# Performance work log

Hardware: AMD Instinct MI355X
Metric: run time of the kernel (lower is better)

The kernel has to match this reference:

```python
import jax, jax.numpy as jnp
import numpy as np

D_MODEL = 1024
N_HEADS = 16
D_HEAD = 64
NEG = -1000000000.0


def setup_inputs() -> dict:
    key = jax.random.key(0)
    k1, k2, k3 = jax.random.split(key, 3)
    B, T = 2, 2048
    x = jax.random.normal(k1, (B, T, D_MODEL), dtype=jnp.float32)
    # qkv_proj: Linear(d_model, 3*H*D, bias=False) -> weight (3*H*D, d_model)
    w_qkv = jax.random.normal(k2, (3 * N_HEADS * D_HEAD, D_MODEL), dtype=jnp.float32) * (D_MODEL ** -0.5)
    # o_proj: Linear(H*D, d_model, bias=False) -> weight (d_model, H*D)
    w_o = jax.random.normal(k3, (D_MODEL, N_HEADS * D_HEAD), dtype=jnp.float32) * ((N_HEADS * D_HEAD) ** -0.5)
    return {"x": x, "w_qkv": w_qkv, "w_o": w_o}


def reference(x, w_qkv, w_o):
    B, T, _ = x.shape
    H, D = N_HEADS, D_HEAD
    scale = D ** -0.5
    qkv = jnp.einsum('btm,nm->btn', x, w_qkv).reshape(B, T, 3, H, D)
    q, k, v = qkv[:, :, 0], qkv[:, :, 1], qkv[:, :, 2]  # (B,T,H,D)
    # scores: (B,H,T,T)
    attn = jnp.einsum('bqhd,bkhd->bhqk', q, k) * scale
    causal = jnp.tril(jnp.ones((T, T), dtype=x.dtype))
    attn = attn + (1.0 - causal) * NEG
    attn = jax.nn.softmax(attn, axis=-1)
    out = jnp.einsum('bhqk,bkhd->bqhd', attn, v).reshape(B, T, H * D)
    out = jnp.einsum('btn,mn->btm', out, w_o)
    return (out, k, v)
```

## Files before the change

### kernel.cpp

```cpp
#include <hip/hip_runtime.h>
#include <cstdint>

typedef unsigned short u16;
typedef __bf16 bf16x8 __attribute__((ext_vector_type(8)));
typedef float f32x4 __attribute__((ext_vector_type(4)));
typedef short s4 __attribute__((ext_vector_type(4)));

#define T_SEQ 2048
#define NH 16

__device__ __forceinline__ u16 f2bf(float f) {
  union { float f; uint32_t u; } x; x.f = f;
  uint32_t r = (x.u + 0x7fffu + ((x.u >> 16) & 1u)) >> 16;
  return (u16)r;
}

__device__ __forceinline__ uint32_t pk2bf(float a, float b) {
  union { float f; uint32_t u; } x, y; x.f = a; y.f = b;
  uint32_t lo = (x.u + 0x7fffu + ((x.u >> 16) & 1u)) >> 16;
  uint32_t hi = (y.u + 0x7fffu + ((y.u >> 16) & 1u)) >> 16;
  return lo | (hi << 16);
}

__device__ __forceinline__ void cvt8(u16* dst, const float* src) {
  float4 a = *(const float4*)src;
  float4 b = *(const float4*)(src + 4);
  uint4 o;
  o.x = pk2bf(a.x, a.y); o.y = pk2bf(a.z, a.w);
  o.z = pk2bf(b.x, b.y); o.w = pk2bf(b.z, b.w);
  *(uint4*)dst = o;
}

__global__ __launch_bounds__(256) void cvt_all(const float* __restrict__ x,
                                               const float* __restrict__ wq,
                                               const float* __restrict__ wo,
                                               u16* __restrict__ dst) {
  int i = blockIdx.x * 256 + threadIdx.x;
  const float* src; int off;
  if (i < 524288)      { src = x;  off = 0; }
  else if (i < 917504) { src = wq; off = 524288; }
  else                 { src = wo; off = 917504; }
  cvt8(&dst[(size_t)i * 8], &src[(size_t)(i - off) * 8]);
}

__device__ __forceinline__ s4 cvt4(f32x4 v) {
  union { __bf16 b[4]; s4 s; } u;
  u.b[0] = (__bf16)v[0]; u.b[1] = (__bf16)v[1];
  u.b[2] = (__bf16)v[2]; u.b[3] = (__bf16)v[3];
  return u.s;
}

__device__ __forceinline__ f32x4 mfma16(s4 a, s4 b, f32x4 c) {
#if __has_builtin(__builtin_amdgcn_mfma_f32_16x16x16bf16_1k)
  return __builtin_amdgcn_mfma_f32_16x16x16bf16_1k(a, b, c, 0, 0, 0);
#else
  asm("v_mfma_f32_16x16x16_bf16 %0, %1, %2, %0" : "+v"(c) : "v"(a), "v"(b));
  return c;
#endif
}

__device__ __forceinline__ float exp2fast(float x) {
#if __has_builtin(__builtin_amdgcn_exp2f)
  return __builtin_amdgcn_exp2f(x);
#else
  float r; asm("v_exp_f32 %0, %1" : "=v"(r) : "v"(x)); return r;
#endif
}

__device__ __forceinline__ void gl_lds(const u16* g, u16* ldsbase) {
  __builtin_amdgcn_global_load_lds(
      (const __attribute__((address_space(1))) void*)g,
      (__attribute__((address_space(3))) void*)ldsbase, 16, 0, 0);
}

template <bool CF32, bool KV, int WAVES>
__global__ __launch_bounds__(WAVES * 64) void gemm_bt(
    const u16* __restrict__ A, const u16* __restrict__ W,
    void* __restrict__ Cp, float* __restrict__ outk, float* __restrict__ outv,
    u16* __restrict__ vtp, int M, int N, int K) {
  constexpr int NJ = (WAVES == 4) ? 4 : 2;
  constexpr int SI = 16 / WAVES;
  __shared__ __align__(16) u16 As[2][128 * 64];
  __shared__ __align__(16) u16 Bs[2][128 * 64];
  const int tid  = threadIdx.x;
  const int bid  = blockIdx.y * gridDim.x + blockIdx.x;
  const int per  = (gridDim.x * gridDim.y) >> 3;
  const int swz  = (bid & 7) * per + (bid >> 3);
  const int n0   = (swz % gridDim.x) * 128;
  const int m0   = (swz / gridDim.x) * 128;
  const int lane = tid & 63;
  const int wave = tid >> 6;
  const int wm   = (WAVES == 4 ? (wave >> 1) : (wave >> 2)) * 64;
  const int wn   = (WAVES == 4 ? (wave & 1) * 64 : (wave & 3) * 32);
  const int l15  = lane & 15;
  const int quad = lane >> 4;
  const int srow = lane >> 3;
  const int sc   = lane & 7;

  f32x4 acc[4][NJ];
#pragma unroll
  for (int i = 0; i < 4; i++)
#pragma unroll
    for (int j = 0; j < NJ; j++) acc[i][j] = (f32x4){0.f, 0.f, 0.f, 0.f};

  auto stage = [&](int d, int k0) {
#pragma unroll
    for (int i = 0; i < SI; i++) {
      int r0  = (i * WAVES + wave) * 8;
      int row = r0 + srow;
      int gc  = (sc ^ (row & 7)) << 3;
      gl_lds(&A[(size_t)(m0 + row) * K + k0 + gc], &As[d][r0 * 64]);
      gl_lds(&W[(size_t)(n0 + row) * K + k0 + gc], &Bs[d][r0 * 64]);
    }
  };

  stage(0, 0);
  asm volatile("s_waitcnt vmcnt(0)" ::: "memory");
  __builtin_amdgcn_s_barrier();
  __builtin_amdgcn_sched_barrier(0);

  const int NT = K >> 6;
  int cur = 0;
  for (int t = 0; t < NT; t++) {
    if (t + 1 < NT) stage(cur ^ 1, (t + 1) * 64);
#pragma unroll
    for (int kk = 0; kk < 64; kk += 32) {
      bf16x8 af[4], bfr[NJ];
#pragma unroll
      for (int i = 0; i < 4; i++) {
        int arow = wm + i * 16 + l15;
        af[i] = *(const bf16x8*)((const char*)&As[cur][0] + arow * 128 +
                                 ((((kk >> 3) + quad) ^ (arow & 7)) << 4));
      }
#pragma unroll
      for (int j = 0; j < NJ; j++) {
        int brow = wn + j * 16 + l15;
        bfr[j] = *(const bf16x8*)((const char*)&Bs[cur][0] + brow * 128 +
                                  ((((kk >> 3) + quad) ^ (brow & 7)) << 4));
      }
#pragma unroll
      for (int i = 0; i < 4; i++)
#pragma unroll
        for (int j = 0; j < NJ; j++)
          acc[i][j] = __builtin_amdgcn_mfma_f32_16x16x32_bf16(af[i], bfr[j], acc[i][j], 0, 0, 0);
    }
    asm volatile("s_waitcnt vmcnt(0)" ::: "memory");
    __builtin_amdgcn_s_barrier();
    __builtin_amdgcn_sched_barrier(0);
    cur ^= 1;
  }
#pragma unroll
  for (int i = 0; i < 4; i++)
#pragma unroll
    for (int j = 0; j < NJ; j++) {
      const int row0 = m0 + wm + i * 16 + quad * 4;
      const int col  = n0 + wn + j * 16 + l15;
      if constexpr (CF32) {
#pragma unroll
        for (int r = 0; r < 4; r++)
          ((float*)Cp)[(size_t)(row0 + r) * N + col] = acc[i][j][r];
      } else if (KV && col >= 2048) {
        const int hd = col - 2048;
        const int b_ = row0 >> 11, t_ = row0 & 2047;
        uint2 pk;
        pk.x = pk2bf(acc[i][j][0], acc[i][j][1]);
        pk.y = pk2bf(acc[i][j][2], acc[i][j][3]);
        *(uint2*)&vtp[((size_t)(b_ * NH + (hd >> 6)) * 64 + (hd & 63)) * 2048 + t_] = pk;
#pragma unroll
        for (int r = 0; r < 4; r++)
          outv[(size_t)(row0 + r) * 1024 + hd] = acc[i][j][r];
      } else {
#pragma unroll
        for (int r = 0; r < 4; r++) {
          float v = acc[i][j][r];
          ((u16*)Cp)[(size_t)(row0 + r) * N + col] = f2bf(v);
          if constexpr (KV) {
            if (col >= 1024) outk[(size_t)(row0 + r) * 1024 + (col - 1024)] = v;
          }
        }
      }
    }
}

__global__ __launch_bounds__(256) void attn(const u16* __restrict__ qkv,
                                            const u16* __restrict__ vt,
                                            u16* __restrict__ o) {
  __shared__ __align__(16) u16 Ks[2][64 * 64];
  __shared__ __align__(16) u16 Vts[2][64 * 64];

  const int tid  = threadIdx.x;
  const int bx   = blockIdx.x;
  const int by   = blockIdx.y;
  const int b    = by >> 4, h = by & 15;
  const int lane = tid & 63, wave = tid >> 6;
  const int l15  = lane & 15, quad = lane >> 4;
  const int srow = lane >> 3, sc = lane & 7;
  const size_t qbase = (size_t)b * T_SEQ * 3072;
  const size_t vbase = (size_t)(b * NH + h) * 64 * 2048;
  const float C = 0.1803368801f;

  const int u  = (bx + (by & 7) * 5) & 31;
  const int c  = by >> 3;
  const int v_ = (u + ((c >> 1) << 4)) & 31;
  const int qt = (c & 1) ? (31 - v_) : v_;
  const int steps = qt + 1;

  const int wq0  = qt * 64 + wave * 16;
  const int qrow = wq0 + l15;

  const u16* qp = &qkv[qbase + (size_t)qrow * 3072 + h * 64];
  const bf16x8 qf0 = *(const bf16x8*)&qp[quad * 8];
  const bf16x8 qf1 = *(const bf16x8*)&qp[32 + quad * 8];

  f32x4 acc_o[4];
#pragma unroll
  for (int n = 0; n < 4; n++) acc_o[n] = (f32x4){0.f, 0.f, 0.f, 0.f};
  float m2run = -1e30f, lrun = 0.f;

  auto stage = [&](int buf, int kt) {
    const int k0 = kt * 64;
#pragma unroll
    for (int i = 0; i < 2; i++) {
      int r0  = (wave * 2 + i) * 8;
      int row = r0 + srow;
      int gc  = (sc ^ (row & 7)) << 3;
      gl_lds(&qkv[qbase + (size_t)(k0 + row) * 3072 + 1024 + h * 64 + gc], &Ks[buf][r0 * 64]);
      gl_lds(&vt[vbase + (size_t)row * 2048 + k0 + gc], &Vts[buf][r0 * 64]);
    }
  };

  stage(0, 0);

  for (int s = 0; s < steps; s++) {
    const int cur = s & 1;
    asm volatile("s_waitcnt vmcnt(0)" ::: "memory");
    __builtin_amdgcn_s_barrier();
    __builtin_amdgcn_sched_barrier(0);

    if (s + 1 < steps) stage(cur ^ 1, s + 1);

    const int k0 = s * 64;

    f32x4 sacc[4];
#pragma unroll
    for (int j = 0; j < 4; j++) sacc[j] = (f32x4){0.f, 0.f, 0.f, 0.f};
    __builtin_amdgcn_s_setprio(1);
#pragma unroll
    for (int j = 0; j < 4; j++) {
      int krow = j * 16 + l15;
      const char* kb = (const char*)&Ks[cur][0] + krow * 128;
      bf16x8 kfa = *(const bf16x8*)(kb + ((quad ^ (krow & 7)) << 4));
      bf16x8 kfb = *(const bf16x8*)(kb + (((4 + quad) ^ (krow & 7)) << 4));
      sacc[j] = __builtin_amdgcn_mfma_f32_16x16x32_bf16(kfa, qf0, sacc[j], 0, 0, 0);
      sacc[j] = __builtin_amdgcn_mfma_f32_16x16x32_bf16(kfb, qf1, sacc[j], 0, 0, 0);
    }
    __builtin_amdgcn_s_setprio(0);

    if (s == qt) {
#pragma unroll
      for (int j = 0; j < 4; j++)
#pragma unroll
        for (int r = 0; r < 4; r++) {
          int k = k0 + j * 16 + quad * 4 + r;
          if (k > qrow) sacc[j][r] = -1e30f;
        }
    }

    float mj[4];
#pragma unroll
    for (int j = 0; j < 4; j++)
      mj[j] = fmaxf(fmaxf(sacc[j][0], sacc[j][1]), fmaxf(sacc[j][2], sacc[j][3]));
    float mx = fmaxf(fmaxf(mj[0], mj[1]), fmaxf(mj[2], mj[3]));
    mx = fmaxf(mx, __shfl_xor(mx, 16));
    mx = fmaxf(mx, __shfl_xor(mx, 32));
    const float m2x = mx * C;

    if (!__all(m2x <= m2run + 8.0f)) {
      const float m2new = fmaxf(m2run, m2x);
      const float alpha = exp2fast(m2run - m2new);
      lrun *= alpha;
      m2run = m2new;
#pragma unroll
      for (int r = 0; r < 4; r++) {
        float ar = __shfl(alpha, quad * 4 + r);
#pragma unroll
        for (int n = 0; n < 4; n++) acc_o[n][r] *= ar;
      }
    }

    const float nm = m2run;
    float ts[4];
#pragma unroll
    for (int j = 0; j < 4; j++) {
#pragma unroll
      for (int r = 0; r < 4; r++) sacc[j][r] = exp2fast(fmaf(sacc[j][r], C, -nm));
      ts[j] = (sacc[j][0] + sacc[j][1]) + (sacc[j][2] + sacc[j][3]);
    }
    float sum = (ts[0] + ts[1]) + (ts[2] + ts[3]);
    sum += __shfl_xor(sum, 16);
    sum += __shfl_xor(sum, 32);
    lrun += sum;

    s4 pa[4];
#pragma unroll
    for (int j = 0; j < 4; j++) pa[j] = cvt4(sacc[j]);

    __builtin_amdgcn_s_setprio(1);
#pragma unroll
    for (int j = 0; j < 4; j++)
#pragma unroll
      for (int n = 0; n < 4; n++) {
        int vrow = n * 16 + l15;
        int ch = (j * 2 + (quad >> 1)) ^ (vrow & 7);
        const s4 vf = *(const s4*)((const char*)&Vts[cur][0] + vrow * 128 +
                                   (ch << 4) + ((quad & 1) << 3));
        acc_o[n] = mfma16(pa[j], vf, acc_o[n]);
      }
    __builtin_amdgcn_s_setprio(0);
  }

  const float linv = 1.0f / lrun;
#pragma unroll
  for (int r = 0; r < 4; r++) {
    const float lr = __shfl(linv, quad * 4 + r);
    const int row = wq0 + quad * 4 + r;
#pragma unroll
    for (int n = 0; n < 4; n++)
      o[(size_t)(b * T_SEQ + row) * 1024 + h * 64 + n * 16 + l15] =
          f2bf(acc_o[n][r] * lr);
  }
}

extern "C" void kernel_launch(void* const* d_in, const int* in_sizes, int n_in,
                              void* d_out, int out_size, void* d_ws, size_t ws_size,
                              hipStream_t stream) {
  const float* x     = (const float*)d_in[0];
  const float* w_qkv = (const float*)d_in[1];
  const float* w_o   = (const float*)d_in[2];
  float* out  = (float*)d_out;
  float* outk = out + (size_t)4194304;
  float* outv = out + (size_t)8388608;

  u16* qkv = (u16*)d_ws;
  u16* vt  = qkv + (size_t)4096 * 3072;
  u16* ao  = vt  + (size_t)4194304;
  u16* xb  = ao  + (size_t)4194304;
  u16* wqb = xb  + (size_t)4194304;
  u16* wob = wqb + (size_t)3145728;

  cvt_all<<<4096, 256, 0, stream>>>(x, w_qkv, w_o, xb);

  gemm_bt<false, true, 4><<<dim3(24, 32), 256, 0, stream>>>(
      xb, wqb, qkv, outk, outv, vt, 4096, 3072, 1024);
  attn<<<dim3(32, 32), 256, 0, stream>>>(qkv, vt, ao);
  gemm_bt<true, false, 8><<<dim3(8, 32), 512, 0, stream>>>(
      ao, wob, out, nullptr, nullptr, nullptr, 4096, 1024, 1024);
}
```

Baseline: 200.3 us.

## Fuse fp32-to-bf16 conversion into GEMM tile loads and drop separate convert kernel

Removes the standalone conversion kernel that turned x, w_qkv and w_o into bf16 workspace copies. The GEMMs now load fp32 tiles into registers, round them to bf16, and write them into swizzled LDS. The QKV GEMM also moves from 4 to 8 waves per block. This saves one launch and the extra write and reread of the bf16 copies. In exchange each GEMM reads twice as many bytes per tile, does the conversion in-kernel, and gives up the async global_load_lds path for fp32 operands. A blocking vmcnt wait plus LDS writes now sit after the MFMA loop.

```diff
diff --git a/kernel.cpp b/kernel.cpp
--- a/kernel.cpp
+++ b/kernel.cpp
@@ -20,27 +20,6 @@
   uint32_t lo = (x.u + 0x7fffu + ((x.u >> 16) & 1u)) >> 16;
   uint32_t hi = (y.u + 0x7fffu + ((y.u >> 16) & 1u)) >> 16;
   return lo | (hi << 16);
-}
-
-__device__ __forceinline__ void cvt8(u16* dst, const float* src) {
-  float4 a = *(const float4*)src;
-  float4 b = *(const float4*)(src + 4);
-  uint4 o;
-  o.x = pk2bf(a.x, a.y); o.y = pk2bf(a.z, a.w);
-  o.z = pk2bf(b.x, b.y); o.w = pk2bf(b.z, b.w);
-  *(uint4*)dst = o;
-}
-
-__global__ __launch_bounds__(256) void cvt_all(const float* __restrict__ x,
-                                               const float* __restrict__ wq,
-                                               const float* __restrict__ wo,
-                                               u16* __restrict__ dst) {
-  int i = blockIdx.x * 256 + threadIdx.x;
-  const float* src; int off;
-  if (i < 524288)      { src = x;  off = 0; }
-  else if (i < 917504) { src = wq; off = 524288; }
-  else                 { src = wo; off = 917504; }
-  cvt8(&dst[(size_t)i * 8], &src[(size_t)(i - off) * 8]);
 }
 
 __device__ __forceinline__ s4 cvt4(f32x4 v) {
@@ -73,13 +52,11 @@
       (__attribute__((address_space(3))) void*)ldsbase, 16, 0, 0);
 }
 
-template <bool CF32, bool KV, int WAVES>
-__global__ __launch_bounds__(WAVES * 64) void gemm_bt(
-    const u16* __restrict__ A, const u16* __restrict__ W,
+template <bool CF32, bool KV, bool A_FP32>
+__global__ __launch_bounds__(512) void gemm_bt(
+    const void* __restrict__ Avp, const float* __restrict__ Wfp,
     void* __restrict__ Cp, float* __restrict__ outk, float* __restrict__ outv,
     u16* __restrict__ vtp, int M, int N, int K) {
-  constexpr int NJ = (WAVES == 4) ? 4 : 2;
-  constexpr int SI = 16 / WAVES;
   __shared__ __align__(16) u16 As[2][128 * 64];
   __shared__ __align__(16) u16 Bs[2][128 * 64];
   const int tid  = threadIdx.x;
@@ -90,42 +67,91 @@
   const int m0   = (swz / gridDim.x) * 128;
   const int lane = tid & 63;
   const int wave = tid >> 6;
-  const int wm   = (WAVES == 4 ? (wave >> 1) : (wave >> 2)) * 64;
-  const int wn   = (WAVES == 4 ? (wave & 1) * 64 : (wave & 3) * 32);
+  const int wm   = (wave >> 2) * 64;
+  const int wn   = (wave & 3) * 32;
   const int l15  = lane & 15;
   const int quad = lane >> 4;
+  const int srw  = wave * 16 + (lane >> 2);
+  const int c0   = lane & 3;
   const int srow = lane >> 3;
   const int sc   = lane & 7;
 
-  f32x4 acc[4][NJ];
+  const float* Afp = (const float*)Avp;
+  const u16*   Ab  = (const u16*)Avp;
+
+  f32x4 acc[4][2];
 #pragma unroll
   for (int i = 0; i < 4; i++)
 #pragma unroll
-    for (int j = 0; j < NJ; j++) acc[i][j] = (f32x4){0.f, 0.f, 0.f, 0.f};
-
-  auto stage = [&](int d, int k0) {
-#pragma unroll
-    for (int i = 0; i < SI; i++) {
-      int r0  = (i * WAVES + wave) * 8;
-      int row = r0 + srow;
-      int gc  = (sc ^ (row & 7)) << 3;
-      gl_lds(&A[(size_t)(m0 + row) * K + k0 + gc], &As[d][r0 * 64]);
-      gl_lds(&W[(size_t)(n0 + row) * K + k0 + gc], &Bs[d][r0 * 64]);
-    }
-  };
-
-  stage(0, 0);
+    for (int j = 0; j < 2; j++) acc[i][j] = (f32x4){0.f, 0.f, 0.f, 0.f};
+
+  float4 ra[4], rw[4];
+
+  auto loadW = [&](int k0) {
+    const float* src = &Wfp[(size_t)(n0 + srw) * K + k0];
+    const int g0 = ((c0)     ^ (srw & 7)) * 8;
+    const int g1 = ((c0 + 4) ^ (srw & 7)) * 8;
+    rw[0] = *(const float4*)(src + g0);
+    rw[1] = *(const float4*)(src + g0 + 4);
+    rw[2] = *(const float4*)(src + g1);
+    rw[3] = *(const float4*)(src + g1 + 4);
+  };
+  auto writeW = [&](int d) {
+    uint4 o;
+    o.x = pk2bf(rw[0].x, rw[0].y); o.y = pk2bf(rw[0].z, rw[0].w);
+    o.z = pk2bf(rw[1].x, rw[1].y); o.w = pk2bf(rw[1].z, rw[1].w);
+    *(uint4*)&Bs[d][srw * 64 + c0 * 8] = o;
+    o.x = pk2bf(rw[2].x, rw[2].y); o.y = pk2bf(rw[2].z, rw[2].w);
+    o.z = pk2bf(rw[3].x, rw[3].y); o.w = pk2bf(rw[3].z, rw[3].w);
+    *(uint4*)&Bs[d][srw * 64 + (c0 + 4) * 8] = o;
+  };
+  auto loadA = [&](int d, int k0) {
+    if constexpr (A_FP32) {
+      const float* src = &Afp[(size_t)(m0 + srw) * K + k0];
+      const int g0 = ((c0)     ^ (srw & 7)) * 8;
+      const int g1 = ((c0 + 4) ^ (srw & 7)) * 8;
+      ra[0] = *(const float4*)(src + g0);
+      ra[1] = *(const float4*)(src + g0 + 4);
+      ra[2] = *(const float4*)(src + g1);
+      ra[3] = *(const float4*)(src + g1 + 4);
+    } else {
+#pragma unroll
+      for (int i = 0; i < 2; i++) {
+        int r0  = (i * 8 + wave) * 8;
+        int row = r0 + srow;
+        int gc  = (sc ^ (row & 7)) << 3;
+        gl_lds(&Ab[(size_t)(m0 + row) * K + k0 + gc], &As[d][r0 * 64]);
+      }
+    }
+  };
+  auto writeA = [&](int d) {
+    if constexpr (A_FP32) {
+      uint4 o;
+      o.x = pk2bf(ra[0].x, ra[0].y); o.y = pk2bf(ra[0].z, ra[0].w);
+      o.z = pk2bf(ra[1].x, ra[1].y); o.w = pk2bf(ra[1].z, ra[1].w);
+      *(uint4*)&As[d][srw * 64 + c0 * 8] = o;
+      o.x = pk2bf(ra[2].x, ra[2].y); o.y = pk2bf(ra[2].z, ra[2].w);
+      o.z = pk2bf(ra[3].x, ra[3].y); o.w = pk2bf(ra[3].z, ra[3].w);
+      *(uint4*)&As[d][srw * 64 + (c0 + 4) * 8] = o;
+    }
+  };
+
+  loadA(0, 0); loadW(0);
   asm volatile("s_waitcnt vmcnt(0)" ::: "memory");
+  __builtin_amdgcn_sched_barrier(0);
+  writeA(0); writeW(0);
+  asm volatile("s_waitcnt lgkmcnt(0)" ::: "memory");
+  __builtin_amdgcn_sched_barrier(0);
   __builtin_amdgcn_s_barrier();
   __builtin_amdgcn_sched_barrier(0);
 
   const int NT = K >> 6;
   int cur = 0;
   for (int t = 0; t < NT; t++) {
-    if (t + 1 < NT) stage(cur ^ 1, (t + 1) * 64);
+    if (t + 1 < NT) { loadA(cur ^ 1, (t + 1) * 64); loadW((t + 1) * 64); }
 #pragma unroll
     for (int kk = 0; kk < 64; kk += 32) {
-      bf16x8 af[4], bfr[NJ];
+      bf16x8 af[4], bfr[2];
 #pragma unroll
       for (int i = 0; i < 4; i++) {
         int arow = wm + i * 16 + l15;
@@ -133,7 +159,7 @@
                                  ((((kk >> 3) + quad) ^ (arow & 7)) << 4));
       }
 #pragma unroll
-      for (int j = 0; j < NJ; j++) {
+      for (int j = 0; j < 2; j++) {
         int brow = wn + j * 16 + l15;
         bfr[j] = *(const bf16x8*)((const char*)&Bs[cur][0] + brow * 128 +
                                   ((((kk >> 3) + quad) ^ (brow & 7)) << 4));
@@ -141,18 +167,25 @@
 #pragma unroll
       for (int i = 0; i < 4; i++)
 #pragma unroll
-        for (int j = 0; j < NJ; j++)
+        for (int j = 0; j < 2; j++)
           acc[i][j] = __builtin_amdgcn_mfma_f32_16x16x32_bf16(af[i], bfr[j], acc[i][j], 0, 0, 0);
     }
-    asm volatile("s_waitcnt vmcnt(0)" ::: "memory");
+    if (t + 1 < NT) {
+      asm volatile("s_waitcnt vmcnt(0)" ::: "memory");
+      __builtin_amdgcn_sched_barrier(0);
+      writeA(cur ^ 1); writeW(cur ^ 1);
+    }
+    asm volatile("s_waitcnt lgkmcnt(0)" ::: "memory");
+    __builtin_amdgcn_sched_barrier(0);
     __builtin_amdgcn_s_barrier();
     __builtin_amdgcn_sched_barrier(0);
     cur ^= 1;
   }
+
 #pragma unroll
   for (int i = 0; i < 4; i++)
 #pragma unroll
-    for (int j = 0; j < NJ; j++) {
+    for (int j = 0; j < 2; j++) {
       const int row0 = m0 + wm + i * 16 + quad * 4;
       const int col  = n0 + wn + j * 16 + l15;
       if constexpr (CF32) {
@@ -344,15 +377,10 @@
   u16* qkv = (u16*)d_ws;
   u16* vt  = qkv + (size_t)4096 * 3072;
   u16* ao  = vt  + (size_t)4194304;
-  u16* xb  = ao  + (size_t)4194304;
-  u16* wqb = xb  + (size_t)4194304;
-  u16* wob = wqb + (size_t)3145728;
-
-  cvt_all<<<4096, 256, 0, stream>>>(x, w_qkv, w_o, xb);
-
-  gemm_bt<false, true, 4><<<dim3(24, 32), 256, 0, stream>>>(
-      xb, wqb, qkv, outk, outv, vt, 4096, 3072, 1024);
+
+  gemm_bt<false, true, true><<<dim3(24, 32), 512, 0, stream>>>(
+      x, w_qkv, qkv, outk, outv, vt, 4096, 3072, 1024);
   attn<<<dim3(32, 32), 256, 0, stream>>>(qkv, vt, ao);
-  gemm_bt<true, false, 8><<<dim3(8, 32), 512, 0, stream>>>(
-      ao, wob, out, nullptr, nullptr, nullptr, 4096, 1024, 1024);
-}
+  gemm_bt<true, false, false><<<dim3(8, 32), 512, 0, stream>>>(
+      ao, w_o, out, nullptr, nullptr, nullptr, 4096, 1024, 1024);
+}
```

Result: slower. 256.5 us (+28.0%).
